# Optimization experiments

Measured on AMD Instinct MI355X. Metric: run time of the kernel, lower is better.

Reference implementation:

```python
import jax, jax.numpy as jnp
import numpy as np

B, K, D = 16384, 20, 256
H = 4                    # attention heads
DECAY = 0.95
THRESH = 2.0             # anomaly z-score threshold
EPS = 1e-8


def setup_inputs() -> dict:
    key = jax.random.key(0)
    ks = jax.random.split(key, 10)
    s = 0.05
    return {
        "storage": jax.random.normal(ks[0], (B, K, D), jnp.float32),
        "new_message": jax.random.normal(ks[1], (B, D), jnp.float32),
        "ad_w1": jax.random.normal(ks[2], (D // 2, D), jnp.float32) * s,
        "ad_b1": jnp.zeros((D // 2,), jnp.float32),
        "ad_w2": jax.random.normal(ks[3], (1, D // 2), jnp.float32) * s,
        "ad_b2": jnp.zeros((1,), jnp.float32),
        "imp_w1": jax.random.normal(ks[4], (D, 2 * D), jnp.float32) * s,
        "imp_b1": jnp.zeros((D,), jnp.float32),
        "imp_w2": jax.random.normal(ks[5], (1, D), jnp.float32) * s,
        "imp_b2": jnp.zeros((1,), jnp.float32),
        "attn_in_w": jax.random.normal(ks[6], (3 * D, D), jnp.float32) * s,
        "attn_in_b": jnp.zeros((3 * D,), jnp.float32),
        "attn_out_w": jax.random.normal(ks[7], (D, D), jnp.float32) * s,
        "attn_out_b": jnp.zeros((D,), jnp.float32),
    }


def reference(storage, new_message, ad_w1, ad_b1, ad_w2, ad_b2,
              imp_w1, imp_b1, imp_w2, imp_b2,
              attn_in_w, attn_in_b, attn_out_w, attn_out_b):
    dt = storage.dtype
    b = storage.shape[0]
    # --- masked historical statistics over the storage slots ---
    mask = (jnp.sum(jnp.abs(storage), axis=-1) > 0).astype(dt)          # [B,K]
    denom = jnp.sum(mask, axis=1, keepdims=True) + EPS                  # [B,1]
    hmean = jnp.sum(storage * mask[..., None], axis=1) / denom          # [B,D]
    diff_sq = ((storage - hmean[:, None, :]) ** 2) * mask[..., None]
    hstd = jnp.sqrt(jnp.sum(diff_sq, axis=1) / denom)                   # [B,D]
    # --- anomaly score: statistical z-score + learned detector ---
    z = jnp.abs((new_message - hmean) / (hstd + EPS))
    stat_anom = jnp.mean((z > THRESH).astype(dt), axis=-1, keepdims=True)  # [B,1]
    h = jax.nn.relu(new_message @ ad_w1.T + ad_b1)
    learned_anom = jax.nn.sigmoid(h @ ad_w2.T + ad_b2)                  # [B,1]
    anomaly = 0.5 * stat_anom + 0.5 * learned_anom
    # --- importance weight ---
    ctx = jnp.concatenate([new_message, hmean], axis=-1)                # [B,2D]
    imp = jax.nn.softplus(jax.nn.relu(ctx @ imp_w1.T + imp_b1) @ imp_w2.T + imp_b2)
    imp = imp * (1.0 + anomaly)                                         # [B,1]
    # --- decay, roll, scatter-insert new message ---
    decay = (DECAY ** jnp.arange(K, dtype=dt))[None, :, None]           # [1,K,1]
    st = storage * decay
    st = jnp.roll(st, shift=1, axis=1)
    st = st.at[:, 0, :].set(new_message * imp)                          # [B,K,D]
    # --- multihead attention: query=new_message, key/value=storage ---
    wq, wk, wv = jnp.split(attn_in_w, 3, axis=0)
    bq, bk, bv = jnp.split(attn_in_b, 3)
    hd = D // H
    q = (new_message @ wq.T + bq).reshape(b, 1, H, hd)
    k = (st @ wk.T + bk).reshape(b, K, H, hd)
    v = (st @ wv.T + bv).reshape(b, K, H, hd)
    scores = jnp.einsum('bqhd,bkhd->bhqk', q, k) / jnp.sqrt(jnp.asarray(hd, dt))
    attn = jax.nn.softmax(scores, axis=-1)                              # [B,H,1,K]
    ctx_out = jnp.einsum('bhqk,bkhd->bqhd', attn, v).reshape(b, 1, D)
    agg = (ctx_out @ attn_out_w.T + attn_out_b)[:, 0, :]                # [B,D]
    return st, agg
```

## Files before the change

### kernel.cpp

```cpp
#include <hip/hip_runtime.h>
#include <hip/hip_bf16.h>
#include <math.h>

#define B_N 16384
#define K_N 20
#define D_N 256
#define H_N 4

typedef __attribute__((ext_vector_type(8))) short v8s;
typedef __attribute__((ext_vector_type(4))) float v4f;
typedef __hip_bfloat16 bf16;

static __device__ __forceinline__ float bf2f(bf16 x){ return __bfloat162float(x); }
static __device__ __forceinline__ bf16 f2bf(float x){ return __float2bfloat16(x); }
static __device__ __forceinline__ float bfb2f(short s){ bf16 v; *(short*)&v = s; return __bfloat162float(v); }
static __device__ __forceinline__ short bfbits(float x){ bf16 v = __float2bfloat16(x); return *(short*)&v; }

__global__ __launch_bounds__(256) void k_prep(
    const float* __restrict__ ad_w1, const float* __restrict__ ad_b1,
    const float* __restrict__ imp_w1, const float* __restrict__ imp_b1,
    const float* __restrict__ attn_in_w, const float* __restrict__ attn_in_b,
    const float* __restrict__ attn_out_w, const float* __restrict__ nm,
    bf16* __restrict__ attn_bf, bf16* __restrict__ w1bT, bf16* __restrict__ wout_bf,
    bf16* __restrict__ wcat, float* __restrict__ catb,
    float* __restrict__ g, float* __restrict__ qc,
    bf16* __restrict__ wkT, bf16* __restrict__ nm_bf)
{
    long o = (long)blockIdx.x * 256 + threadIdx.x;
    const long n_attn = 768*256, n_w1b = 65536, n_wout = 256*256, n_wcat = 640*256;
    const long n_catb = 640, n_g = 1024, n_qc = 4, n_wkT = 1024*64, n_nm = (long)B_N*256;
    if (o < n_attn){ attn_bf[o] = f2bf(attn_in_w[o]); return; } o -= n_attn;
    if (o < n_w1b){
        int k = (int)(o >> 8), j = (int)(o & 255);
        w1bT[o] = f2bf(imp_w1[j*512 + 256 + k]); return; } o -= n_w1b;
    if (o < n_wout){ wout_bf[o] = f2bf(attn_out_w[o]); return; } o -= n_wout;
    if (o < n_wcat){
        int r = (int)(o >> 8), c = (int)(o & 255); float v;
        if (r < 128)      v = ad_w1[r*256 + c];
        else if (r < 384) v = attn_in_w[(r-128)*256 + c];
        else              v = imp_w1[(r-384)*512 + c];
        wcat[o] = f2bf(v); return; } o -= n_wcat;
    if (o < n_catb){
        int r = (int)o; float v;
        if (r < 128) v = ad_b1[r]; else if (r < 384) v = attn_in_b[r-128]; else v = imp_b1[r-384];
        catb[r] = v; return; } o -= n_catb;
    if (o < n_g){
        int h = (int)(o >> 8), d = (int)(o & 255); float s = 0.f;
        for (int j = 0; j < 64; ++j) s += attn_in_w[(h*64+j)*256 + d] * attn_in_b[256 + h*64 + j];
        g[o] = s; return; } o -= n_g;
    if (o < n_qc){
        int h = (int)o; float s = 0.f;
        for (int j = 0; j < 64; ++j) s += attn_in_b[h*64+j] * attn_in_b[256 + h*64 + j];
        qc[h] = s; return; } o -= n_qc;
    if (o < n_wkT){
        int c = (int)(o >> 6), i = (int)(o & 63);
        int h = c >> 8, d = c & 255;
        wkT[o] = f2bf(attn_in_w[(256 + h*64 + i)*256 + d]); return; } o -= n_wkT;
    if (o < n_nm){ nm_bf[o] = f2bf(nm[o]); return; }
}

__global__ __launch_bounds__(256) void k_gemm(
    const bf16* __restrict__ X, int ldx, int agshift, int agstride,
    const bf16* __restrict__ W, int ldw,
    const float* __restrict__ bias,
    const bf16* __restrict__ csrc, int ldc,
    void* __restrict__ outp, int ldo, int out_bf16,
    int relu_hi, int Kd)
{
    int wave = threadIdx.x >> 6, lane = threadIdx.x & 63;
    int l15 = lane & 15, koct = lane >> 4;
    int rblk = blockIdx.x * 64 + wave * 16;
    int cb = blockIdx.y * 64;
    long arow = rblk + l15;
    long aoff = (long)(cb >> agshift) * agstride;
    const bf16* Xp = X + arow * ldx + aoff + koct * 8;
    v4f acc[4];
    #pragma unroll
    for (int ct = 0; ct < 4; ++ct) acc[ct] = (v4f){0.f,0.f,0.f,0.f};
    for (int k0 = 0; k0 < Kd; k0 += 32){
        v8s a = *(const v8s*)(Xp + k0);
        #pragma unroll
        for (int ct = 0; ct < 4; ++ct){
            const bf16* Wp = W + (long)(cb + ct*16 + l15) * ldw + k0 + koct * 8;
            v8s bb = *(const v8s*)Wp;
            acc[ct] = __builtin_amdgcn_mfma_f32_16x16x32_bf16(a, bb, acc[ct], 0, 0, 0);
        }
    }
    int orow_base = rblk + koct * 4;
    #pragma unroll
    for (int ct = 0; ct < 4; ++ct){
        int ocol = cb + ct*16 + l15;
        float bv = bias ? bias[ocol] : 0.0f;
        #pragma unroll
        for (int r = 0; r < 4; ++r){
            long orow = orow_base + r;
            float v = acc[ct][r] + bv;
            if (csrc) v += bf2f(csrc[orow * ldc + ocol]);
            if (ocol < relu_hi) v = fmaxf(v, 0.0f);
            if (out_bf16) ((bf16*)outp)[orow * ldo + ocol] = f2bf(v);
            else          ((float*)outp)[orow * ldo + ocol] = v;
        }
    }
}

__global__ __launch_bounds__(256, 4) void k_fused(
    const float* __restrict__ storage, const float* __restrict__ nm,
    const bf16* __restrict__ R_bf, const bf16* __restrict__ cat1,
    const bf16* __restrict__ w1bT,
    const float* __restrict__ ad_w2, const float* __restrict__ ad_b2,
    const float* __restrict__ imp_w2, const float* __restrict__ imp_b2,
    const float* __restrict__ g, const float* __restrict__ qc,
    float* __restrict__ st_out, bf16* __restrict__ u_bf)
{
    __shared__ float4 stor4[K_N * 64];
    __shared__ float nm_s[D_N];
    __shared__ float mu_s[D_N];
    __shared__ float redm[4 * D_N];
    __shared__ float mask_s[K_N];
    __shared__ int   zc_s[H_N];
    __shared__ float red_s[2*H_N];
    int b = blockIdx.x, t = threadIdx.x, h = t >> 6, lane = t & 63;
    const float4* S4 = (const float4*)(storage + (long)b * K_N * D_N);
    float4*       O4 = (float4*)(st_out + (long)b * K_N * D_N);

    float4 nm4 = ((const float4*)(nm + (long)b * D_N))[lane];

    float4 vv[5];
    #pragma unroll
    for (int j = 0; j < 5; ++j) vv[j] = S4[t + j*256];
    if (h == 0) ((float4*)nm_s)[lane] = nm4;
    {
        float dd = 1.0f;
        #pragma unroll
        for (int j = 0; j < 3; ++j) if (j < h) dd *= 0.95f;
        const float step = 0.81450625f;
        #pragma unroll
        for (int j = 0; j < 5; ++j){
            int i = t + j*256;
            int row = h + 4*j;
            stor4[i] = vv[j];
            bool nz = (vv[j].x != 0.f) || (vv[j].y != 0.f) || (vv[j].z != 0.f) || (vv[j].w != 0.f);
            unsigned long long bal = __ballot(nz);
            if (lane == 0) mask_s[row] = (bal != 0ULL) ? 1.0f : 0.0f;
            if (row < K_N-1){
                float4 o;
                o.x = vv[j].x * dd; o.y = vv[j].y * dd;
                o.z = vv[j].z * dd; o.w = vv[j].w * dd;
                O4[i + 64] = o;
            }
            dd *= step;
        }
    }
    __syncthreads();

    {
        const float* S = (const float*)stor4;
        float cm = 0.f, s1 = 0.f, s2 = 0.f;
        #pragma unroll
        for (int k = 0; k < K_N; ++k){
            float m = mask_s[k];
            float x = S[k*D_N + t];
            cm += m; s1 += m*x; s2 += m*x*x;
        }
        float denom = cm + 1e-8f;
        float mu = s1 / denom;
        float var = (s2 - 2.0f*mu*s1 + mu*mu*cm) / denom;
        float sd = sqrtf(fmaxf(var, 0.0f));
        mu_s[t] = mu;
        float z = fabsf((nm_s[t] - mu) / (sd + 1e-8f));
        unsigned long long bal = __ballot(z > 2.0f);
        if (lane == 0) zc_s[h] = __popcll(bal);
    }
    __syncthreads();

    float pre1a = bf2f(cat1[(long)b*640 + 384 + t]);
    {
        float ax = 0.f, ay = 0.f, az = 0.f, aw = 0.f;
        const bf16* wp = w1bT + (long)(h*64)*256 + 4*lane;
        #pragma unroll 4
        for (int s = 0; s < 64; ++s){
            ushort4 wv = *(const ushort4*)(wp + s*256);
            float m = mu_s[h*64 + s];
            ax += m * bfb2f((short)wv.x);
            ay += m * bfb2f((short)wv.y);
            az += m * bfb2f((short)wv.z);
            aw += m * bfb2f((short)wv.w);
        }
        float4 a4; a4.x = ax; a4.y = ay; a4.z = az; a4.w = aw;
        ((float4*)redm)[h*64 + lane] = a4;
    }
    __syncthreads();

    {
        float acc = pre1a + redm[t] + redm[256+t] + redm[512+t] + redm[768+t];
        float tj = fmaxf(acc, 0.0f);
        float pi = tj * imp_w2[t];
        float pl = (t < 128) ? bf2f(cat1[(long)b*640 + t]) * ad_w2[t] : 0.0f;
        #pragma unroll
        for (int s = 32; s; s >>= 1){ pi += __shfl_xor(pi, s); pl += __shfl_xor(pl, s); }
        if (lane == 0){ red_s[h] = pi; red_s[H_N + h] = pl; }
    }
    __syncthreads();

    float impv;
    {
        float p  = red_s[0]+red_s[1]+red_s[2]+red_s[3] + imp_b2[0];
        float plr= red_s[4]+red_s[5]+red_s[6]+red_s[7] + ad_b2[0];
        float learned = 1.0f / (1.0f + expf(-plr));
        float stat = (float)(zc_s[0]+zc_s[1]+zc_s[2]+zc_s[3]) * (1.0f/256.0f);
        float sp = (p > 20.0f) ? p : log1pf(expf(p));
        impv = sp * (1.0f + 0.5f*stat + 0.5f*learned);
    }
    if (h == 0){
        float4 o;
        o.x = impv * nm4.x; o.y = impv * nm4.y;
        o.z = impv * nm4.z; o.w = impv * nm4.w;
        O4[lane] = o;
    }

    short4 r4  = ((const short4*)(R_bf + (long)b * (H_N*D_N) + h * D_N))[lane];
    float4 R4;
    R4.x = bfb2f(r4.x); R4.y = bfb2f(r4.y); R4.z = bfb2f(r4.z); R4.w = bfb2f(r4.w);
    float4 g4 = ((const float4*)(g + h * D_N))[lane];

    const int NP = K_N + 1;
    float p[NP];
    p[0] = nm4.x*g4.x + nm4.y*g4.y + nm4.z*g4.z + nm4.w*g4.w;
    p[1] = nm4.x*R4.x + nm4.y*R4.y + nm4.z*R4.z + nm4.w*R4.w;
    #pragma unroll
    for (int k = 0; k < K_N-1; ++k){
        float4 x = stor4[k*64 + lane];
        p[2+k] = x.x*R4.x + x.y*R4.y + x.z*R4.z + x.w*R4.w;
    }
    #pragma unroll
    for (int s = 32; s; s >>= 1){
        #pragma unroll
        for (int j = 0; j < NP; ++j) p[j] += __shfl_xor(p[j], s);
    }
    float qb = p[0] + qc[h];
    float s0 = (impv * p[1] + qb) * 0.125f;
    float mx = s0;
    {
        float dd = 1.0f;
        #pragma unroll
        for (int k = 0; k < K_N-1; ++k){
            p[2+k] = (dd * p[2+k] + qb) * 0.125f;
            mx = fmaxf(mx, p[2+k]);
            dd *= 0.95f;
        }
    }
    float w0 = expf(s0 - mx);
    float l = w0;
    #pragma unroll
    for (int k = 0; k < K_N-1; ++k){ p[2+k] = expf(p[2+k] - mx); l += p[2+k]; }
    float inv = 1.0f / l;
    w0 *= inv * impv;

    float4 acc;
    acc.x = w0 * nm4.x; acc.y = w0 * nm4.y; acc.z = w0 * nm4.z; acc.w = w0 * nm4.w;
    {
        float dd = inv;
        #pragma unroll
        for (int k = 0; k < K_N-1; ++k){
            float c = p[2+k] * dd;
            float4 x = stor4[k*64 + lane];
            acc.x += c*x.x; acc.y += c*x.y; acc.z += c*x.z; acc.w += c*x.w;
            dd *= 0.95f;
        }
    }
    short4 us;
    us.x = bfbits(acc.x); us.y = bfbits(acc.y); us.z = bfbits(acc.z); us.w = bfbits(acc.w);
    ((short4*)(u_bf + (long)b * (H_N*D_N) + h * D_N))[lane] = us;
}

extern "C" void kernel_launch(void* const* d_in, const int* in_sizes, int n_in,
                              void* d_out, int out_size, void* d_ws, size_t ws_size,
                              hipStream_t stream)
{
    (void)in_sizes; (void)n_in; (void)out_size; (void)ws_size;
    const float* storage    = (const float*)d_in[0];
    const float* nm         = (const float*)d_in[1];
    const float* ad_w1      = (const float*)d_in[2];
    const float* ad_b1      = (const float*)d_in[3];
    const float* ad_w2      = (const float*)d_in[4];
    const float* ad_b2      = (const float*)d_in[5];
    const float* imp_w1     = (const float*)d_in[6];
    const float* imp_b1     = (const float*)d_in[7];
    const float* imp_w2     = (const float*)d_in[8];
    const float* imp_b2     = (const float*)d_in[9];
    const float* attn_in_w  = (const float*)d_in[10];
    const float* attn_in_b  = (const float*)d_in[11];
    const float* attn_out_w = (const float*)d_in[12];
    const float* attn_out_b = (const float*)d_in[13];

    char* p = (char*)d_ws;
    auto alloc = [&](size_t bytes)->char*{ char* r = p; p += (bytes + 255) & ~(size_t)255; return r; };
    bf16*  attn_bf   = (bf16*) alloc((size_t)768*256*2);
    bf16*  w1bT      = (bf16*) alloc((size_t)256*256*2);
    bf16*  wout_bf   = (bf16*) alloc((size_t)256*256*2);
    bf16*  wcat      = (bf16*) alloc((size_t)640*256*2);
    float* catb      = (float*)alloc((size_t)640*4);
    float* g         = (float*)alloc((size_t)1024*4);
    float* qc        = (float*)alloc((size_t)4*4);
    bf16*  wkT       = (bf16*) alloc((size_t)1024*64*2);
    bf16*  nm_bf     = (bf16*) alloc((size_t)B_N*256*2);
    bf16*  cat1      = (bf16*) alloc((size_t)B_N*640*2);
    bf16*  R_bf      = (bf16*) alloc((size_t)B_N*1024*2);
    bf16*  u_bf      = (bf16*) alloc((size_t)B_N*1024*2);
    bf16*  ctx_bf    = (bf16*) alloc((size_t)B_N*256*2);

    float* st_out  = (float*)d_out;
    float* agg_out = (float*)d_out + (size_t)B_N * K_N * D_N;

    {
        long total = 768*256 + 65536 + 256*256 + 640*256 + 640 + 1024 + 4 + 1024*64 + (long)B_N*256;
        int grid = (int)((total + 255) / 256);
        k_prep<<<grid, 256, 0, stream>>>(ad_w1, ad_b1, imp_w1, imp_b1, attn_in_w, attn_in_b,
                                         attn_out_w, nm, attn_bf, w1bT, wout_bf, wcat, catb,
                                         g, qc, wkT, nm_bf);
    }
    k_gemm<<<dim3(B_N/64, 640/64), 256, 0, stream>>>(nm_bf, 256, 30, 0, wcat, 256, catb,
        (const bf16*)nullptr, 0, cat1, 640, 1, 128, 256);
    k_gemm<<<dim3(B_N/64, 1024/64), 256, 0, stream>>>(cat1 + 128, 640, 8, 64, wkT, 64,
        (const float*)nullptr, (const bf16*)nullptr, 0, R_bf, 1024, 1, 0, 64);
    k_fused<<<B_N, 256, 0, stream>>>(storage, nm, R_bf, cat1, w1bT,
        ad_w2, ad_b2, imp_w2, imp_b2, g, qc, st_out, u_bf);
    k_gemm<<<dim3(B_N/64, 256/64), 256, 0, stream>>>(u_bf, 1024, 6, 256, attn_bf + 512*256, 256,
        attn_in_b + 512, (const bf16*)nullptr, 0, ctx_bf, 256, 1, 0, 256);
    k_gemm<<<dim3(B_N/64, 256/64), 256, 0, stream>>>(ctx_bf, 256, 30, 0, wout_bf, 256,
        attn_out_b, (const bf16*)nullptr, 0, agg_out, 256, 0, 0, 256);
}
```

Before: 874.8 us.

## Fold query/key and value/output weight products into precomputed fused matrices

Precomputes Aw = Wq_h^T·Wk_h and Wm = Wout·Wv_h per head, so the per-query key-projection GEMM reads new_message directly and the value and output projections merge into one K=1024 GEMM. This drops one GEMM launch, the ctx_bf intermediate, and the q columns of the first GEMM. It also raises k_fused occupancy bounds and reuses shared memory for nm_s. The trade-off is a larger prep kernel doing 64-term dot products per element, and a K=256 rather than K=64 score GEMM.

```diff
diff --git a/kernel.cpp b/kernel.cpp
--- a/kernel.cpp
+++ b/kernel.cpp
@@ -20,30 +20,29 @@
     const float* __restrict__ ad_w1, const float* __restrict__ ad_b1,
     const float* __restrict__ imp_w1, const float* __restrict__ imp_b1,
     const float* __restrict__ attn_in_w, const float* __restrict__ attn_in_b,
-    const float* __restrict__ attn_out_w, const float* __restrict__ nm,
-    bf16* __restrict__ attn_bf, bf16* __restrict__ w1bT, bf16* __restrict__ wout_bf,
-    bf16* __restrict__ wcat, float* __restrict__ catb,
+    const float* __restrict__ attn_out_w, const float* __restrict__ attn_out_b,
+    const float* __restrict__ nm,
+    bf16* __restrict__ w1bT, bf16* __restrict__ wcat, float* __restrict__ catb,
     float* __restrict__ g, float* __restrict__ qc,
-    bf16* __restrict__ wkT, bf16* __restrict__ nm_bf)
+    bf16* __restrict__ Aw, float* __restrict__ beta,
+    bf16* __restrict__ Wm, float* __restrict__ cagg,
+    bf16* __restrict__ nm_bf)
 {
     long o = (long)blockIdx.x * 256 + threadIdx.x;
-    const long n_attn = 768*256, n_w1b = 65536, n_wout = 256*256, n_wcat = 640*256;
-    const long n_catb = 640, n_g = 1024, n_qc = 4, n_wkT = 1024*64, n_nm = (long)B_N*256;
-    if (o < n_attn){ attn_bf[o] = f2bf(attn_in_w[o]); return; } o -= n_attn;
-    if (o < n_w1b){
+    const long n_w1bT = 65536, n_wcat = 384*256, n_catb = 384, n_g = 1024, n_qc = 4;
+    const long n_Aw = 262144, n_beta = 1024, n_Wm = 262144, n_cagg = 256;
+    const long n_nm = (long)B_N*256;
+    if (o < n_w1bT){
         int k = (int)(o >> 8), j = (int)(o & 255);
-        w1bT[o] = f2bf(imp_w1[j*512 + 256 + k]); return; } o -= n_w1b;
-    if (o < n_wout){ wout_bf[o] = f2bf(attn_out_w[o]); return; } o -= n_wout;
+        w1bT[o] = f2bf(imp_w1[j*512 + 256 + k]); return; } o -= n_w1bT;
     if (o < n_wcat){
         int r = (int)(o >> 8), c = (int)(o & 255); float v;
-        if (r < 128)      v = ad_w1[r*256 + c];
-        else if (r < 384) v = attn_in_w[(r-128)*256 + c];
-        else              v = imp_w1[(r-384)*512 + c];
+        if (r < 128) v = ad_w1[r*256 + c];
+        else         v = imp_w1[(r-128)*512 + c];
         wcat[o] = f2bf(v); return; } o -= n_wcat;
     if (o < n_catb){
-        int r = (int)o; float v;
-        if (r < 128) v = ad_b1[r]; else if (r < 384) v = attn_in_b[r-128]; else v = imp_b1[r-384];
-        catb[r] = v; return; } o -= n_catb;
+        int r = (int)o;
+        catb[r] = (r < 128) ? ad_b1[r] : imp_b1[r-128]; return; } o -= n_catb;
     if (o < n_g){
         int h = (int)(o >> 8), d = (int)(o & 255); float s = 0.f;
         for (int j = 0; j < 64; ++j) s += attn_in_w[(h*64+j)*256 + d] * attn_in_b[256 + h*64 + j];
@@ -52,10 +51,27 @@
         int h = (int)o; float s = 0.f;
         for (int j = 0; j < 64; ++j) s += attn_in_b[h*64+j] * attn_in_b[256 + h*64 + j];
         qc[h] = s; return; } o -= n_qc;
-    if (o < n_wkT){
-        int c = (int)(o >> 6), i = (int)(o & 63);
-        int h = c >> 8, d = c & 255;
-        wkT[o] = f2bf(attn_in_w[(256 + h*64 + i)*256 + d]); return; } o -= n_wkT;
+    if (o < n_Aw){
+        int c = (int)(o >> 8), e = (int)(o & 255);
+        int h = c >> 8, d = c & 255; float s = 0.f;
+        for (int i = 0; i < 64; ++i)
+            s += attn_in_w[(h*64+i)*256 + e] * attn_in_w[(256 + h*64 + i)*256 + d];
+        Aw[o] = f2bf(s); return; } o -= n_Aw;
+    if (o < n_beta){
+        int c = (int)o; int h = c >> 8, d = c & 255; float s = 0.f;
+        for (int i = 0; i < 64; ++i)
+            s += attn_in_b[h*64+i] * attn_in_w[(256 + h*64 + i)*256 + d];
+        beta[c] = s; return; } o -= n_beta;
+    if (o < n_Wm){
+        int i = (int)(o >> 10), k = (int)(o & 1023);
+        int h = k >> 8, d = k & 255; float s = 0.f;
+        for (int jj = 0; jj < 64; ++jj)
+            s += attn_in_w[(512 + h*64 + jj)*256 + d] * attn_out_w[i*256 + h*64 + jj];
+        Wm[o] = f2bf(s); return; } o -= n_Wm;
+    if (o < n_cagg){
+        int i = (int)o; float s = attn_out_b[i];
+        for (int j = 0; j < 256; ++j) s += attn_in_b[512+j] * attn_out_w[i*256 + j];
+        cagg[i] = s; return; } o -= n_cagg;
     if (o < n_nm){ nm_bf[o] = f2bf(nm[o]); return; }
 }
 
@@ -103,7 +119,7 @@
     }
 }
 
-__global__ __launch_bounds__(256, 4) void k_fused(
+__global__ __launch_bounds__(256, 6) void k_fused(
     const float* __restrict__ storage, const float* __restrict__ nm,
     const bf16* __restrict__ R_bf, const bf16* __restrict__ cat1,
     const bf16* __restrict__ w1bT,
@@ -113,12 +129,12 @@
     float* __restrict__ st_out, bf16* __restrict__ u_bf)
 {
     __shared__ float4 stor4[K_N * 64];
-    __shared__ float nm_s[D_N];
+    __shared__ float redm[4 * D_N];
     __shared__ float mu_s[D_N];
-    __shared__ float redm[4 * D_N];
     __shared__ float mask_s[K_N];
     __shared__ int   zc_s[H_N];
     __shared__ float red_s[2*H_N];
+    float* nm_s = redm;
     int b = blockIdx.x, t = threadIdx.x, h = t >> 6, lane = t & 63;
     const float4* S4 = (const float4*)(storage + (long)b * K_N * D_N);
     float4*       O4 = (float4*)(st_out + (long)b * K_N * D_N);
@@ -173,7 +189,7 @@
     }
     __syncthreads();
 
-    float pre1a = bf2f(cat1[(long)b*640 + 384 + t]);
+    float pre1a = bf2f(cat1[(long)b*384 + 128 + t]);
     {
         float ax = 0.f, ay = 0.f, az = 0.f, aw = 0.f;
         const bf16* wp = w1bT + (long)(h*64)*256 + 4*lane;
@@ -195,7 +211,7 @@
         float acc = pre1a + redm[t] + redm[256+t] + redm[512+t] + redm[768+t];
         float tj = fmaxf(acc, 0.0f);
         float pi = tj * imp_w2[t];
-        float pl = (t < 128) ? bf2f(cat1[(long)b*640 + t]) * ad_w2[t] : 0.0f;
+        float pl = (t < 128) ? bf2f(cat1[(long)b*384 + t]) * ad_w2[t] : 0.0f;
         #pragma unroll
         for (int s = 32; s; s >>= 1){ pi += __shfl_xor(pi, s); pl += __shfl_xor(pl, s); }
         if (lane == 0){ red_s[h] = pi; red_s[H_N + h] = pl; }
@@ -295,38 +311,36 @@
 
     char* p = (char*)d_ws;
     auto alloc = [&](size_t bytes)->char*{ char* r = p; p += (bytes + 255) & ~(size_t)255; return r; };
-    bf16*  attn_bf   = (bf16*) alloc((size_t)768*256*2);
     bf16*  w1bT      = (bf16*) alloc((size_t)256*256*2);
-    bf16*  wout_bf   = (bf16*) alloc((size_t)256*256*2);
-    bf16*  wcat      = (bf16*) alloc((size_t)640*256*2);
-    float* catb      = (float*)alloc((size_t)640*4);
+    bf16*  wcat      = (bf16*) alloc((size_t)384*256*2);
+    float* catb      = (float*)alloc((size_t)384*4);
     float* g         = (float*)alloc((size_t)1024*4);
     float* qc        = (float*)alloc((size_t)4*4);
-    bf16*  wkT       = (bf16*) alloc((size_t)1024*64*2);
+    bf16*  Aw        = (bf16*) alloc((size_t)1024*256*2);
+    float* beta      = (float*)alloc((size_t)1024*4);
+    bf16*  Wm        = (bf16*) alloc((size_t)256*1024*2);
+    float* cagg      = (float*)alloc((size_t)256*4);
     bf16*  nm_bf     = (bf16*) alloc((size_t)B_N*256*2);
-    bf16*  cat1      = (bf16*) alloc((size_t)B_N*640*2);
+    bf16*  cat1      = (bf16*) alloc((size_t)B_N*384*2);
     bf16*  R_bf      = (bf16*) alloc((size_t)B_N*1024*2);
     bf16*  u_bf      = (bf16*) alloc((size_t)B_N*1024*2);
-    bf16*  ctx_bf    = (bf16*) alloc((size_t)B_N*256*2);
 
     float* st_out  = (float*)d_out;
     float* agg_out = (float*)d_out + (size_t)B_N * K_N * D_N;
 
     {
-        long total = 768*256 + 65536 + 256*256 + 640*256 + 640 + 1024 + 4 + 1024*64 + (long)B_N*256;
+        long total = 65536 + 384*256 + 384 + 1024 + 4 + 262144 + 1024 + 262144 + 256 + (long)B_N*256;
         int grid = (int)((total + 255) / 256);
         k_prep<<<grid, 256, 0, stream>>>(ad_w1, ad_b1, imp_w1, imp_b1, attn_in_w, attn_in_b,
-                                         attn_out_w, nm, attn_bf, w1bT, wout_bf, wcat, catb,
-                                         g, qc, wkT, nm_bf);
-    }
-    k_gemm<<<dim3(B_N/64, 640/64), 256, 0, stream>>>(nm_bf, 256, 30, 0, wcat, 256, catb,
-        (const bf16*)nullptr, 0, cat1, 640, 1, 128, 256);
-    k_gemm<<<dim3(B_N/64, 1024/64), 256, 0, stream>>>(cat1 + 128, 640, 8, 64, wkT, 64,
-        (const float*)nullptr, (const bf16*)nullptr, 0, R_bf, 1024, 1, 0, 64);
+                                         attn_out_w, attn_out_b, nm,
+                                         w1bT, wcat, catb, g, qc, Aw, beta, Wm, cagg, nm_bf);
+    }
+    k_gemm<<<dim3(B_N/64, 384/64), 256, 0, stream>>>(nm_bf, 256, 30, 0, wcat, 256, catb,
+        (const bf16*)nullptr, 0, cat1, 384, 1, 128, 256);
+    k_gemm<<<dim3(B_N/64, 1024/64), 256, 0, stream>>>(nm_bf, 256, 30, 0, Aw, 256, beta,
+        (const bf16*)nullptr, 0, R_bf, 1024, 1, 0, 256);
     k_fused<<<B_N, 256, 0, stream>>>(storage, nm, R_bf, cat1, w1bT,
         ad_w2, ad_b2, imp_w2, imp_b2, g, qc, st_out, u_bf);
-    k_gemm<<<dim3(B_N/64, 256/64), 256, 0, stream>>>(u_bf, 1024, 6, 256, attn_bf + 512*256, 256,
-        attn_in_b + 512, (const bf16*)nullptr, 0, ctx_bf, 256, 1, 0, 256);
-    k_gemm<<<dim3(B_N/64, 256/64), 256, 0, stream>>>(ctx_bf, 256, 30, 0, wout_bf, 256,
-        attn_out_b, (const bf16*)nullptr, 0, agg_out, 256, 0, 0, 256);
+    k_gemm<<<dim3(B_N/64, 256/64), 256, 0, stream>>>(u_bf, 1024, 30, 0, Wm, 1024, cagg,
+        (const bf16*)nullptr, 0, agg_out, 256, 0, 0, 1024);
 }
```

Result: slower. 933.6 us (+6.7%).

## Restructure fused kernel to one wavefront per batch row with register-held storage

Applied to the files above, without the earlier changes.

The fused per-row kernel now maps one 64-lane wavefront to each batch row instead of a 256-thread block. The 20 storage rows stay in registers rather than LDS, which removes most __syncthreads barriers and shared-memory traffic, and each wave loops over the 4 heads itself. It also adds nontemporal stores for the large st output and fast __expf in the softmax. In exchange, register pressure rises (launch bounds drop to 3 blocks per SM) and each wave redoes the full 256-wide mu·W matvec serially, which can cost latency and occupancy.

```diff
diff --git a/kernel.cpp b/kernel.cpp
--- a/kernel.cpp
+++ b/kernel.cpp
@@ -15,6 +15,14 @@
 static __device__ __forceinline__ bf16 f2bf(float x){ return __float2bfloat16(x); }
 static __device__ __forceinline__ float bfb2f(short s){ bf16 v; *(short*)&v = s; return __bfloat162float(v); }
 static __device__ __forceinline__ short bfbits(float x){ bf16 v = __float2bfloat16(x); return *(short*)&v; }
+static __device__ __forceinline__ float4 bf4f(ushort4 a){
+    float4 r; r.x = bfb2f((short)a.x); r.y = bfb2f((short)a.y);
+    r.z = bfb2f((short)a.z); r.w = bfb2f((short)a.w); return r;
+}
+static __device__ __forceinline__ void nt_store4(float4 o, float4* p){
+    v4f ov; ov[0] = o.x; ov[1] = o.y; ov[2] = o.z; ov[3] = o.w;
+    __builtin_nontemporal_store(ov, (v4f*)p);
+}
 
 __global__ __launch_bounds__(256) void k_prep(
     const float* __restrict__ ad_w1, const float* __restrict__ ad_b1,
@@ -103,7 +111,7 @@
     }
 }
 
-__global__ __launch_bounds__(256, 4) void k_fused(
+__global__ __launch_bounds__(256, 3) void k_wave(
     const float* __restrict__ storage, const float* __restrict__ nm,
     const bf16* __restrict__ R_bf, const bf16* __restrict__ cat1,
     const bf16* __restrict__ w1bT,
@@ -112,165 +120,146 @@
     const float* __restrict__ g, const float* __restrict__ qc,
     float* __restrict__ st_out, bf16* __restrict__ u_bf)
 {
-    __shared__ float4 stor4[K_N * 64];
-    __shared__ float nm_s[D_N];
-    __shared__ float mu_s[D_N];
-    __shared__ float redm[4 * D_N];
-    __shared__ float mask_s[K_N];
-    __shared__ int   zc_s[H_N];
-    __shared__ float red_s[2*H_N];
-    int b = blockIdx.x, t = threadIdx.x, h = t >> 6, lane = t & 63;
-    const float4* S4 = (const float4*)(storage + (long)b * K_N * D_N);
-    float4*       O4 = (float4*)(st_out + (long)b * K_N * D_N);
-
-    float4 nm4 = ((const float4*)(nm + (long)b * D_N))[lane];
-
-    float4 vv[5];
+    __shared__ float mu_lds[4][D_N];
+    int w = threadIdx.x >> 6, lane = threadIdx.x & 63;
+    long b = (long)blockIdx.x * 4 + w;
+    const float4* S4 = (const float4*)(storage + b * K_N * D_N);
+    float4*       O4 = (float4*)(st_out + b * K_N * D_N);
+
+    float4 rows[K_N];
     #pragma unroll
-    for (int j = 0; j < 5; ++j) vv[j] = S4[t + j*256];
-    if (h == 0) ((float4*)nm_s)[lane] = nm4;
+    for (int k = 0; k < K_N; ++k) rows[k] = S4[k*64 + lane];
+    float4 nm4 = ((const float4*)(nm + b * D_N))[lane];
+
+    float cm = 0.f;
+    float4 s1 = {0.f,0.f,0.f,0.f}, s2 = {0.f,0.f,0.f,0.f};
     {
         float dd = 1.0f;
         #pragma unroll
-        for (int j = 0; j < 3; ++j) if (j < h) dd *= 0.95f;
-        const float step = 0.81450625f;
-        #pragma unroll
-        for (int j = 0; j < 5; ++j){
-            int i = t + j*256;
-            int row = h + 4*j;
-            stor4[i] = vv[j];
-            bool nz = (vv[j].x != 0.f) || (vv[j].y != 0.f) || (vv[j].z != 0.f) || (vv[j].w != 0.f);
-            unsigned long long bal = __ballot(nz);
-            if (lane == 0) mask_s[row] = (bal != 0ULL) ? 1.0f : 0.0f;
-            if (row < K_N-1){
-                float4 o;
-                o.x = vv[j].x * dd; o.y = vv[j].y * dd;
-                o.z = vv[j].z * dd; o.w = vv[j].w * dd;
-                O4[i + 64] = o;
+        for (int k = 0; k < K_N; ++k){
+            float4 x = rows[k];
+            bool nz = (x.x != 0.f) || (x.y != 0.f) || (x.z != 0.f) || (x.w != 0.f);
+            float m = (__ballot(nz) != 0ULL) ? 1.0f : 0.0f;
+            cm += m;
+            s1.x += m*x.x; s1.y += m*x.y; s1.z += m*x.z; s1.w += m*x.w;
+            s2.x += m*x.x*x.x; s2.y += m*x.y*x.y; s2.z += m*x.z*x.z; s2.w += m*x.w*x.w;
+            if (k < K_N-1){
+                float4 o; o.x = x.x*dd; o.y = x.y*dd; o.z = x.z*dd; o.w = x.w*dd;
+                nt_store4(o, &O4[(k+1)*64 + lane]);
             }
-            dd *= step;
-        }
-    }
-    __syncthreads();
-
-    {
-        const float* S = (const float*)stor4;
-        float cm = 0.f, s1 = 0.f, s2 = 0.f;
-        #pragma unroll
-        for (int k = 0; k < K_N; ++k){
-            float m = mask_s[k];
-            float x = S[k*D_N + t];
-            cm += m; s1 += m*x; s2 += m*x*x;
-        }
-        float denom = cm + 1e-8f;
-        float mu = s1 / denom;
-        float var = (s2 - 2.0f*mu*s1 + mu*mu*cm) / denom;
-        float sd = sqrtf(fmaxf(var, 0.0f));
-        mu_s[t] = mu;
-        float z = fabsf((nm_s[t] - mu) / (sd + 1e-8f));
-        unsigned long long bal = __ballot(z > 2.0f);
-        if (lane == 0) zc_s[h] = __popcll(bal);
-    }
-    __syncthreads();
-
-    float pre1a = bf2f(cat1[(long)b*640 + 384 + t]);
-    {
-        float ax = 0.f, ay = 0.f, az = 0.f, aw = 0.f;
-        const bf16* wp = w1bT + (long)(h*64)*256 + 4*lane;
+            dd *= 0.95f;
+        }
+    }
+    float denom = cm + 1e-8f;
+    float4 mu;
+    mu.x = s1.x/denom; mu.y = s1.y/denom; mu.z = s1.z/denom; mu.w = s1.w/denom;
+    float stat;
+    {
+        float vx = (s2.x - 2.f*mu.x*s1.x + mu.x*mu.x*cm)/denom;
+        float vy = (s2.y - 2.f*mu.y*s1.y + mu.y*mu.y*cm)/denom;
+        float vz = (s2.z - 2.f*mu.z*s1.z + mu.z*mu.z*cm)/denom;
+        float vw = (s2.w - 2.f*mu.w*s1.w + mu.w*mu.w*cm)/denom;
+        float sx = sqrtf(fmaxf(vx,0.f)) + 1e-8f, sy = sqrtf(fmaxf(vy,0.f)) + 1e-8f;
+        float sz = sqrtf(fmaxf(vz,0.f)) + 1e-8f, sw = sqrtf(fmaxf(vw,0.f)) + 1e-8f;
+        int zc = __popcll(__ballot(fabsf((nm4.x-mu.x)/sx) > 2.0f))
+               + __popcll(__ballot(fabsf((nm4.y-mu.y)/sy) > 2.0f))
+               + __popcll(__ballot(fabsf((nm4.z-mu.z)/sz) > 2.0f))
+               + __popcll(__ballot(fabsf((nm4.w-mu.w)/sw) > 2.0f));
+        stat = (float)zc * (1.0f/256.0f);
+    }
+    ((float4*)mu_lds[w])[lane] = mu;
+
+    float4 y = {0.f,0.f,0.f,0.f};
+    {
+        const bf16* wp = w1bT + 4*lane;
         #pragma unroll 4
-        for (int s = 0; s < 64; ++s){
-            ushort4 wv = *(const ushort4*)(wp + s*256);
-            float m = mu_s[h*64 + s];
-            ax += m * bfb2f((short)wv.x);
-            ay += m * bfb2f((short)wv.y);
-            az += m * bfb2f((short)wv.z);
-            aw += m * bfb2f((short)wv.w);
-        }
-        float4 a4; a4.x = ax; a4.y = ay; a4.z = az; a4.w = aw;
-        ((float4*)redm)[h*64 + lane] = a4;
-    }
-    __syncthreads();
-
-    {
-        float acc = pre1a + redm[t] + redm[256+t] + redm[512+t] + redm[768+t];
-        float tj = fmaxf(acc, 0.0f);
-        float pi = tj * imp_w2[t];
-        float pl = (t < 128) ? bf2f(cat1[(long)b*640 + t]) * ad_w2[t] : 0.0f;
+        for (int k0 = 0; k0 < 64; ++k0){
+            float4 m4 = ((const float4*)mu_lds[w])[k0];
+            float4 f0 = bf4f(*(const ushort4*)(wp + (4*k0+0)*256));
+            float4 f1 = bf4f(*(const ushort4*)(wp + (4*k0+1)*256));
+            float4 f2 = bf4f(*(const ushort4*)(wp + (4*k0+2)*256));
+            float4 f3 = bf4f(*(const ushort4*)(wp + (4*k0+3)*256));
+            y.x += m4.x*f0.x + m4.y*f1.x + m4.z*f2.x + m4.w*f3.x;
+            y.y += m4.x*f0.y + m4.y*f1.y + m4.z*f2.y + m4.w*f3.y;
+            y.z += m4.x*f0.z + m4.y*f1.z + m4.z*f2.z + m4.w*f3.z;
+            y.w += m4.x*f0.w + m4.y*f1.w + m4.z*f2.w + m4.w*f3.w;
+        }
+    }
+
+    float impv;
+    {
+        short4 pr = ((const short4*)(cat1 + b*640 + 384))[lane];
+        float4 w2 = ((const float4*)imp_w2)[lane];
+        float tx = fmaxf(bfb2f(pr.x) + y.x, 0.f), ty = fmaxf(bfb2f(pr.y) + y.y, 0.f);
+        float tz = fmaxf(bfb2f(pr.z) + y.z, 0.f), tw = fmaxf(bfb2f(pr.w) + y.w, 0.f);
+        float pi = tx*w2.x + ty*w2.y + tz*w2.z + tw*w2.w;
+        float pl = bf2f(cat1[b*640 + lane]) * ad_w2[lane]
+                 + bf2f(cat1[b*640 + 64 + lane]) * ad_w2[64 + lane];
         #pragma unroll
         for (int s = 32; s; s >>= 1){ pi += __shfl_xor(pi, s); pl += __shfl_xor(pl, s); }
-        if (lane == 0){ red_s[h] = pi; red_s[H_N + h] = pl; }
-    }
-    __syncthreads();
-
-    float impv;
-    {
-        float p  = red_s[0]+red_s[1]+red_s[2]+red_s[3] + imp_b2[0];
-        float plr= red_s[4]+red_s[5]+red_s[6]+red_s[7] + ad_b2[0];
-        float learned = 1.0f / (1.0f + expf(-plr));
-        float stat = (float)(zc_s[0]+zc_s[1]+zc_s[2]+zc_s[3]) * (1.0f/256.0f);
-        float sp = (p > 20.0f) ? p : log1pf(expf(p));
+        float learned = 1.0f / (1.0f + expf(-(pl + ad_b2[0])));
+        float pp = pi + imp_b2[0];
+        float sp = (pp > 20.0f) ? pp : log1pf(expf(pp));
         impv = sp * (1.0f + 0.5f*stat + 0.5f*learned);
     }
-    if (h == 0){
-        float4 o;
-        o.x = impv * nm4.x; o.y = impv * nm4.y;
-        o.z = impv * nm4.z; o.w = impv * nm4.w;
-        O4[lane] = o;
-    }
-
-    short4 r4  = ((const short4*)(R_bf + (long)b * (H_N*D_N) + h * D_N))[lane];
-    float4 R4;
-    R4.x = bfb2f(r4.x); R4.y = bfb2f(r4.y); R4.z = bfb2f(r4.z); R4.w = bfb2f(r4.w);
-    float4 g4 = ((const float4*)(g + h * D_N))[lane];
-
-    const int NP = K_N + 1;
-    float p[NP];
-    p[0] = nm4.x*g4.x + nm4.y*g4.y + nm4.z*g4.z + nm4.w*g4.w;
-    p[1] = nm4.x*R4.x + nm4.y*R4.y + nm4.z*R4.z + nm4.w*R4.w;
-    #pragma unroll
-    for (int k = 0; k < K_N-1; ++k){
-        float4 x = stor4[k*64 + lane];
-        p[2+k] = x.x*R4.x + x.y*R4.y + x.z*R4.z + x.w*R4.w;
-    }
-    #pragma unroll
-    for (int s = 32; s; s >>= 1){
-        #pragma unroll
-        for (int j = 0; j < NP; ++j) p[j] += __shfl_xor(p[j], s);
-    }
-    float qb = p[0] + qc[h];
-    float s0 = (impv * p[1] + qb) * 0.125f;
-    float mx = s0;
-    {
-        float dd = 1.0f;
+    {
+        float4 o; o.x = impv*nm4.x; o.y = impv*nm4.y; o.z = impv*nm4.z; o.w = impv*nm4.w;
+        nt_store4(o, &O4[lane]);
+    }
+
+    const bf16* Rb = R_bf + b * (H_N*D_N);
+    #pragma unroll 1
+    for (int h = 0; h < H_N; ++h){
+        short4 r4 = ((const short4*)(Rb + h*D_N))[lane];
+        float4 R4 = bf4f(*(ushort4*)&r4);
+        float4 g4 = ((const float4*)(g + h*D_N))[lane];
+        float p[K_N+1];
+        p[0] = nm4.x*g4.x + nm4.y*g4.y + nm4.z*g4.z + nm4.w*g4.w;
+        p[1] = nm4.x*R4.x + nm4.y*R4.y + nm4.z*R4.z + nm4.w*R4.w;
         #pragma unroll
         for (int k = 0; k < K_N-1; ++k){
-            p[2+k] = (dd * p[2+k] + qb) * 0.125f;
-            mx = fmaxf(mx, p[2+k]);
-            dd *= 0.95f;
-        }
-    }
-    float w0 = expf(s0 - mx);
-    float l = w0;
-    #pragma unroll
-    for (int k = 0; k < K_N-1; ++k){ p[2+k] = expf(p[2+k] - mx); l += p[2+k]; }
-    float inv = 1.0f / l;
-    w0 *= inv * impv;
-
-    float4 acc;
-    acc.x = w0 * nm4.x; acc.y = w0 * nm4.y; acc.z = w0 * nm4.z; acc.w = w0 * nm4.w;
-    {
-        float dd = inv;
-        #pragma unroll
-        for (int k = 0; k < K_N-1; ++k){
-            float c = p[2+k] * dd;
-            float4 x = stor4[k*64 + lane];
-            acc.x += c*x.x; acc.y += c*x.y; acc.z += c*x.z; acc.w += c*x.w;
-            dd *= 0.95f;
-        }
-    }
-    short4 us;
-    us.x = bfbits(acc.x); us.y = bfbits(acc.y); us.z = bfbits(acc.z); us.w = bfbits(acc.w);
-    ((short4*)(u_bf + (long)b * (H_N*D_N) + h * D_N))[lane] = us;
+            float4 x = rows[k];
+            p[2+k] = x.x*R4.x + x.y*R4.y + x.z*R4.z + x.w*R4.w;
+        }
+        #pragma unroll
+        for (int s = 32; s; s >>= 1){
+            #pragma unroll
+            for (int j = 0; j < K_N+1; ++j) p[j] += __shfl_xor(p[j], s);
+        }
+        float qb = p[0] + qc[h];
+        float s0 = (impv * p[1] + qb) * 0.125f;
+        float mx = s0;
+        {
+            float dd = 1.0f;
+            #pragma unroll
+            for (int k = 0; k < K_N-1; ++k){
+                p[2+k] = (dd * p[2+k] + qb) * 0.125f;
+                mx = fmaxf(mx, p[2+k]);
+                dd *= 0.95f;
+            }
+        }
+        float w0 = __expf(s0 - mx);
+        float l = w0;
+        #pragma unroll
+        for (int k = 0; k < K_N-1; ++k){ p[2+k] = __expf(p[2+k] - mx); l += p[2+k]; }
+        float inv = 1.0f / l;
+        w0 *= inv * impv;
+        float4 acc;
+        acc.x = w0*nm4.x; acc.y = w0*nm4.y; acc.z = w0*nm4.z; acc.w = w0*nm4.w;
+        {
+            float dd = inv;
+            #pragma unroll
+            for (int k = 0; k < K_N-1; ++k){
+                float c = p[2+k] * dd;
+                float4 x = rows[k];
+                acc.x += c*x.x; acc.y += c*x.y; acc.z += c*x.z; acc.w += c*x.w;
+                dd *= 0.95f;
+            }
+        }
+        short4 us;
+        us.x = bfbits(acc.x); us.y = bfbits(acc.y); us.z = bfbits(acc.z); us.w = bfbits(acc.w);
+        ((short4*)(u_bf + b*(H_N*D_N) + h*D_N))[lane] = us;
+    }
 }
 
 extern "C" void kernel_launch(void* const* d_in, const int* in_sizes, int n_in,
@@ -323,7 +312,7 @@
         (const bf16*)nullptr, 0, cat1, 640, 1, 128, 256);
     k_gemm<<<dim3(B_N/64, 1024/64), 256, 0, stream>>>(cat1 + 128, 640, 8, 64, wkT, 64,
         (const float*)nullptr, (const bf16*)nullptr, 0, R_bf, 1024, 1, 0, 64);
-    k_fused<<<B_N, 256, 0, stream>>>(storage, nm, R_bf, cat1, w1bT,
+    k_wave<<<B_N/4, 256, 0, stream>>>(storage, nm, R_bf, cat1, w1bT,
         ad_w2, ad_b2, imp_w2, imp_b2, g, qc, st_out, u_bf);
     k_gemm<<<dim3(B_N/64, 256/64), 256, 0, stream>>>(u_bf, 1024, 6, 256, attn_bf + 512*256, 256,
         attn_in_b + 512, (const bf16*)nullptr, 0, ctx_bf, 256, 1, 0, 256);
```

Result: slower. 893.6 us (+2.2%).

## Add wider-tile GEMM variant and raise fused kernel occupancy via shared-memory aliasing

Applied to the files above, without the earlier changes.

Adds k_gemm2, which computes 128 output columns per block (8 MFMA column tiles per wave) so each A fragment is reused across twice as many columns. Three of the GEMM launches switch to it, halving their grid's y dimension. k_fused drops its separate nm_s buffer by aliasing it onto redm and raises its launch bound from 4 to 6 blocks per CU. The aim is fewer redundant A loads and higher occupancy in the fused kernel, at the cost of more accumulator registers in k_gemm2 and possible spills in k_fused under the tighter register budget.

```diff
diff --git a/kernel.cpp b/kernel.cpp
--- a/kernel.cpp
+++ b/kernel.cpp
@@ -103,7 +103,49 @@
     }
 }
 
-__global__ __launch_bounds__(256, 4) void k_fused(
+__global__ __launch_bounds__(256) void k_gemm2(
+    const bf16* __restrict__ X, int ldx, int agshift, int agstride,
+    const bf16* __restrict__ W, int ldw,
+    const float* __restrict__ bias,
+    void* __restrict__ outp, int ldo, int out_bf16,
+    int relu_hi, int Kd)
+{
+    int wave = threadIdx.x >> 6, lane = threadIdx.x & 63;
+    int l15 = lane & 15, koct = lane >> 4;
+    int rblk = blockIdx.x * 64 + wave * 16;
+    int cb = blockIdx.y * 128;
+    long arow = rblk + l15;
+    long aoff = (long)(cb >> agshift) * agstride;
+    const bf16* Xp = X + arow * ldx + aoff + koct * 8;
+    v4f acc[8];
+    #pragma unroll
+    for (int ct = 0; ct < 8; ++ct) acc[ct] = (v4f){0.f,0.f,0.f,0.f};
+    for (int k0 = 0; k0 < Kd; k0 += 32){
+        v8s a = *(const v8s*)(Xp + k0);
+        #pragma unroll
+        for (int ct = 0; ct < 8; ++ct){
+            const bf16* Wp = W + (long)(cb + ct*16 + l15) * ldw + k0 + koct * 8;
+            v8s bb = *(const v8s*)Wp;
+            acc[ct] = __builtin_amdgcn_mfma_f32_16x16x32_bf16(a, bb, acc[ct], 0, 0, 0);
+        }
+    }
+    int orow_base = rblk + koct * 4;
+    #pragma unroll
+    for (int ct = 0; ct < 8; ++ct){
+        int ocol = cb + ct*16 + l15;
+        float bv = bias ? bias[ocol] : 0.0f;
+        #pragma unroll
+        for (int r = 0; r < 4; ++r){
+            long orow = orow_base + r;
+            float v = acc[ct][r] + bv;
+            if (ocol < relu_hi) v = fmaxf(v, 0.0f);
+            if (out_bf16) ((bf16*)outp)[orow * ldo + ocol] = f2bf(v);
+            else          ((float*)outp)[orow * ldo + ocol] = v;
+        }
+    }
+}
+
+__global__ __launch_bounds__(256, 6) void k_fused(
     const float* __restrict__ storage, const float* __restrict__ nm,
     const bf16* __restrict__ R_bf, const bf16* __restrict__ cat1,
     const bf16* __restrict__ w1bT,
@@ -113,12 +155,12 @@
     float* __restrict__ st_out, bf16* __restrict__ u_bf)
 {
     __shared__ float4 stor4[K_N * 64];
-    __shared__ float nm_s[D_N];
+    __shared__ float redm[4 * D_N];
     __shared__ float mu_s[D_N];
-    __shared__ float redm[4 * D_N];
     __shared__ float mask_s[K_N];
     __shared__ int   zc_s[H_N];
     __shared__ float red_s[2*H_N];
+    float* nm_s = redm;
     int b = blockIdx.x, t = threadIdx.x, h = t >> 6, lane = t & 63;
     const float4* S4 = (const float4*)(storage + (long)b * K_N * D_N);
     float4*       O4 = (float4*)(st_out + (long)b * K_N * D_N);
@@ -319,14 +361,14 @@
                                          attn_out_w, nm, attn_bf, w1bT, wout_bf, wcat, catb,
                                          g, qc, wkT, nm_bf);
     }
-    k_gemm<<<dim3(B_N/64, 640/64), 256, 0, stream>>>(nm_bf, 256, 30, 0, wcat, 256, catb,
-        (const bf16*)nullptr, 0, cat1, 640, 1, 128, 256);
-    k_gemm<<<dim3(B_N/64, 1024/64), 256, 0, stream>>>(cat1 + 128, 640, 8, 64, wkT, 64,
-        (const float*)nullptr, (const bf16*)nullptr, 0, R_bf, 1024, 1, 0, 64);
+    k_gemm2<<<dim3(B_N/64, 640/128), 256, 0, stream>>>(nm_bf, 256, 30, 0, wcat, 256, catb,
+        cat1, 640, 1, 128, 256);
+    k_gemm2<<<dim3(B_N/64, 1024/128), 256, 0, stream>>>(cat1 + 128, 640, 8, 64, wkT, 64,
+        (const float*)nullptr, R_bf, 1024, 1, 0, 64);
     k_fused<<<B_N, 256, 0, stream>>>(storage, nm, R_bf, cat1, w1bT,
         ad_w2, ad_b2, imp_w2, imp_b2, g, qc, st_out, u_bf);
     k_gemm<<<dim3(B_N/64, 256/64), 256, 0, stream>>>(u_bf, 1024, 6, 256, attn_bf + 512*256, 256,
         attn_in_b + 512, (const bf16*)nullptr, 0, ctx_bf, 256, 1, 0, 256);
-    k_gemm<<<dim3(B_N/64, 256/64), 256, 0, stream>>>(ctx_bf, 256, 30, 0, wout_bf, 256,
-        attn_out_b, (const bf16*)nullptr, 0, agg_out, 256, 0, 0, 256);
-}
+    k_gemm2<<<dim3(B_N/64, 256/128), 256, 0, stream>>>(ctx_bf, 256, 30, 0, wout_bf, 256,
+        attn_out_b, agg_out, 256, 0, 0, 256);
+}
```

Result: faster. 850.7 us (-2.7%).
